# Kernel optimization log

Hardware: AMD Instinct MI355X
Metric: run time of the kernel (lower is better)

## Reference

```python
import jax, jax.numpy as jnp
import numpy as np
import math

B, S, D, H, FF, V, L = 8, 1024, 512, 8, 2048, 32000, 6
HD = D // H
EPS = 1e-6


def _positional_encoding(seq_len, d_model):
    pos = np.arange(seq_len, dtype=np.float32)[:, None]
    div = np.exp(np.arange(0, d_model, 2, dtype=np.float32) * (-math.log(10000.0) / d_model))
    pe = np.zeros((seq_len, d_model), dtype=np.float32)
    pe[:, 0::2] = np.sin(pos * div)
    pe[:, 1::2] = np.cos(pos * div)
    return jnp.asarray(pe)[None]  # [1, S, D]


def setup_inputs() -> dict:
    key = jax.random.key(0)
    ks = jax.random.split(key, 10)
    s = 0.02
    return {
        'tokens': jax.random.randint(ks[0], (B, S), 0, V, dtype=jnp.int32),
        'mask': jnp.ones((B, 1, 1, S), dtype=jnp.int32),
        'emb': jax.random.normal(ks[1], (V, D), jnp.float32) * s,
        'Wq': jax.random.normal(ks[2], (D, D), jnp.float32) * s,
        'bq': jnp.zeros((D,), jnp.float32),
        'Wk': jax.random.normal(ks[3], (D, D), jnp.float32) * s,
        'bk': jnp.zeros((D,), jnp.float32),
        'Wv': jax.random.normal(ks[4], (D, D), jnp.float32) * s,
        'bv': jnp.zeros((D,), jnp.float32),
        'Wo': jax.random.normal(ks[5], (D, D), jnp.float32) * s,
        'bo': jnp.zeros((D,), jnp.float32),
        'W1': jax.random.normal(ks[6], (D, FF), jnp.float32) * s,
        'b1': jnp.zeros((FF,), jnp.float32),
        'W2': jax.random.normal(ks[7], (FF, D), jnp.float32) * s,
        'b2': jnp.zeros((D,), jnp.float32),
        'ln_a1': jnp.ones((1,), jnp.float32),
        'ln_b1': jnp.zeros((1,), jnp.float32),
        'ln_a2': jnp.ones((1,), jnp.float32),
        'ln_b2': jnp.zeros((1,), jnp.float32),
    }


def _layernorm(x, alpha, bias):
    # custom LN from source: unbiased std (torch default), scalar alpha/bias,
    # eps added to std (not variance)
    mean = jnp.mean(x, axis=-1, keepdims=True)
    std = jnp.std(x, axis=-1, keepdims=True, ddof=1)
    return alpha * (x - mean) / (std + EPS) + bias


def reference(tokens, mask, emb, Wq, bq, Wk, bk, Wv, bv, Wo, bo,
              W1, b1, W2, b2, ln_a1, ln_b1, ln_a2, ln_b2):
    b, s = tokens.shape
    x = emb[tokens] * jnp.asarray(math.sqrt(D), emb.dtype)  # [B,S,D]
    x = x + _positional_encoding(s, D)
    neg = jnp.asarray(-1e9, x.dtype)
    scale = jnp.asarray(1.0 / math.sqrt(HD), x.dtype)
    # NOTE: source reuses the same EncoderBlock instance -> shared weights per layer
    for _ in range(L):
        # --- self-attention sublayer (pre-norm residual) ---
        h = _layernorm(x, ln_a1, ln_b1)
        q = (h @ Wq + bq).reshape(b, s, H, HD).transpose(0, 2, 1, 3)
        k = (h @ Wk + bk).reshape(b, s, H, HD).transpose(0, 2, 1, 3)
        v = (h @ Wv + bv).reshape(b, s, H, HD).transpose(0, 2, 1, 3)
        scores = jnp.einsum('bhqd,bhkd->bhqk', q, k) * scale
        scores = jnp.where(mask == 0, neg, scores)
        attn = jax.nn.softmax(scores, axis=-1)
        o = jnp.einsum('bhqk,bhkd->bhqd', attn, v)
        o = o.transpose(0, 2, 1, 3).reshape(b, s, D)
        x = x + (o @ Wo + bo)
        # --- feed-forward sublayer (pre-norm residual) ---
        h2 = _layernorm(x, ln_a2, ln_b2)
        x = x + (jax.nn.relu(h2 @ W1 + b1) @ W2 + b2)
    return x
```

## Files before the change

kernel.cpp:

```cpp
#include <hip/hip_runtime.h>
#include <hip/hip_bf16.h>
#include <math.h>

#define BB 8
#define SS 1024
#define DD 512
#define HH 8
#define FF 2048
#define LL 6
#define HD 64
#define MM (BB * SS)
#define EPS 1e-6f
#define QKVS 1536

typedef __attribute__((ext_vector_type(8))) short bf16x8;
typedef __attribute__((ext_vector_type(4))) float f32x4;

typedef __attribute__((address_space(1))) const unsigned int g_u32;
typedef __attribute__((address_space(3))) unsigned int l_u32;

__device__ __forceinline__ short f2bf(float f) {
    union { float f; unsigned u; } c; c.f = f;
    unsigned u = c.u;
    u += 0x7fff + ((u >> 16) & 1);
    return (short)(u >> 16);
}

__device__ __forceinline__ void gload_lds16(const void* g, void* l) {
    __builtin_amdgcn_global_load_lds((g_u32*)g, (l_u32*)l, 16, 0, 0);
}

__global__ __launch_bounds__(256) void embed_pe_kernel(
    const int* __restrict__ tokens, const float* __restrict__ emb,
    float* __restrict__ x)
{
    int idx = blockIdx.x * 256 + threadIdx.x;
    int d  = idx & (DD - 1);
    int bs = idx >> 9;
    int s  = bs & (SS - 1);
    int tok = tokens[bs];
    float val = emb[(size_t)tok * DD + d] * 22.62741699796952f;
    int i2 = d & ~1;
    float freq = expf((float)i2 * -0.017988946039015984f);
    float ang = (float)s * freq;
    val += (d & 1) ? cosf(ang) : sinf(ang);
    x[idx] = val;
}

__global__ __launch_bounds__(256) void wcvt_kernel(
    const float* __restrict__ W, short* __restrict__ Wt, int K, int N)
{
    __shared__ float tile[32][33];
    int n0 = blockIdx.x * 32, k0 = blockIdx.y * 32;
    int tx = threadIdx.x & 31, ty = threadIdx.x >> 5;
    #pragma unroll
    for (int i = 0; i < 4; ++i)
        tile[ty + i * 8][tx] = W[(size_t)(k0 + ty + i * 8) * N + n0 + tx];
    __syncthreads();
    #pragma unroll
    for (int i = 0; i < 4; ++i)
        Wt[(size_t)(n0 + ty + i * 8) * K + k0 + tx] = f2bf(tile[tx][ty + i * 8]);
}

__global__ __launch_bounds__(256) void bcat_kernel(
    const float* __restrict__ bq, const float* __restrict__ bk,
    const float* __restrict__ bv, float* __restrict__ out)
{
    int i = blockIdx.x * 256 + threadIdx.x;
    float v = (i < 512) ? bq[i] : (i < 1024 ? bk[i - 512] : bv[i - 1024]);
    out[i] = v;
}

__global__ __launch_bounds__(256) void ln_kernel(
    const float* __restrict__ x, short* __restrict__ y,
    const float* __restrict__ alpha_p, const float* __restrict__ beta_p)
{
    int t = threadIdx.x;
    int half = t >> 7, i = t & 127;
    int row = blockIdx.x * 2 + half;
    const float* xr = x + (size_t)row * DD;
    float4 v = *(const float4*)(xr + i * 4);

    __shared__ float red[8];
    float s = v.x + v.y + v.z + v.w;
    #pragma unroll
    for (int o = 32; o >= 1; o >>= 1) s += __shfl_xor(s, o, 64);
    int wv = t >> 6;
    if ((t & 63) == 0) red[wv] = s;
    __syncthreads();
    float mean = (red[half * 2] + red[half * 2 + 1]) * (1.0f / 512.0f);

    float d0 = v.x - mean, d1 = v.y - mean, d2 = v.z - mean, d3 = v.w - mean;
    float q = d0 * d0 + d1 * d1 + d2 * d2 + d3 * d3;
    #pragma unroll
    for (int o = 32; o >= 1; o >>= 1) q += __shfl_xor(q, o, 64);
    if ((t & 63) == 0) red[4 + wv] = q;
    __syncthreads();
    float var = (red[4 + half * 2] + red[5 + half * 2]) * (1.0f / 511.0f);
    float stdv = sqrtf(var);

    float alpha = alpha_p[0], beta = beta_p[0];
    float inv = alpha / (stdv + EPS);
    short4 ov;
    ov.x = f2bf(d0 * inv + beta); ov.y = f2bf(d1 * inv + beta);
    ov.z = f2bf(d2 * inv + beta); ov.w = f2bf(d3 * inv + beta);
    *(short4*)(y + (size_t)row * DD + i * 4) = ov;
}

template <int BN, bool RELU, bool RES, bool OUT_BF16>
__global__ __launch_bounds__(256) void gemm_mfma(
    const short* __restrict__ A, const short* __restrict__ Wt,
    const float* __restrict__ bias, const float* __restrict__ R,
    void* __restrict__ Cout, int M, int N, int K)
{
    __shared__ __align__(16) short As[128 * 64];
    __shared__ __align__(16) short Bs[BN * 64];

    constexpr int MI = (BN == 128) ? 4 : 2;
    constexpr int NI = 4;

    const int t = threadIdx.x;
    const int w = t >> 6, l = t & 63;
    const int l15 = l & 15, l4 = l >> 4;
    const int wrow = (BN == 128) ? (w >> 1) * 64 : w * 32;
    const int wcol = (BN == 128) ? (w & 1) * 64 : 0;

    const int m0 = blockIdx.y * 128, n0 = blockIdx.x * BN;

    f32x4 acc[MI][NI];
    #pragma unroll
    for (int mi = 0; mi < MI; ++mi)
        #pragma unroll
        for (int ni = 0; ni < NI; ++ni) acc[mi][ni] = (f32x4){0.f, 0.f, 0.f, 0.f};

    const int lrow = l >> 3;
    const int lcol = (l & 7) * 8;

    for (int k0 = 0; k0 < K; k0 += 64) {
        #pragma unroll
        for (int i = 0; i < 4; ++i) {
            int r0 = (w * 4 + i) * 8;
            gload_lds16(A + (size_t)(m0 + r0 + lrow) * K + k0 + lcol, &As[r0 * 64]);
        }
        #pragma unroll
        for (int i = 0; i < BN / 32; ++i) {
            int r0 = (w * (BN / 32) + i) * 8;
            gload_lds16(Wt + (size_t)(n0 + r0 + lrow) * K + k0 + lcol, &Bs[r0 * 64]);
        }
        __syncthreads();

        #pragma unroll
        for (int ks = 0; ks < 2; ++ks) {
            bf16x8 af[MI], bf_[NI];
            #pragma unroll
            for (int mi = 0; mi < MI; ++mi)
                af[mi] = *(const bf16x8*)&As[(wrow + mi * 16 + l15) * 64 + ks * 32 + l4 * 8];
            #pragma unroll
            for (int ni = 0; ni < NI; ++ni)
                bf_[ni] = *(const bf16x8*)&Bs[(wcol + ni * 16 + l15) * 64 + ks * 32 + l4 * 8];
            #pragma unroll
            for (int mi = 0; mi < MI; ++mi)
                #pragma unroll
                for (int ni = 0; ni < NI; ++ni)
                    acc[mi][ni] = __builtin_amdgcn_mfma_f32_16x16x32_bf16(
                        af[mi], bf_[ni], acc[mi][ni], 0, 0, 0);
        }
        __syncthreads();
    }

    #pragma unroll
    for (int mi = 0; mi < MI; ++mi) {
        #pragma unroll
        for (int ni = 0; ni < NI; ++ni) {
            int col = n0 + wcol + ni * 16 + l15;
            float bcol = bias[col];
            #pragma unroll
            for (int r = 0; r < 4; ++r) {
                int row = m0 + wrow + mi * 16 + l4 * 4 + r;
                float c = acc[mi][ni][r] + bcol;
                if (RES)  c += R[(size_t)row * N + col];
                if (RELU) c = fmaxf(c, 0.0f);
                if (OUT_BF16) ((short*)Cout)[(size_t)row * N + col] = f2bf(c);
                else          ((float*)Cout)[(size_t)row * N + col] = c;
            }
        }
    }
}

#define SWZ(row, col) (((row) * 64 + (col)) ^ (((row) & 7) << 3))

__global__ __launch_bounds__(512, 4) void attn_mfma_kernel(
    const short* __restrict__ qkv, const int* __restrict__ mask,
    short* __restrict__ o)
{
    __shared__ __align__(16) short Ks[64 * 64];
    __shared__ __align__(16) short Vt[64 * 64];
    __shared__ __align__(16) short Ps[8][16 * 64];

    const int qt = blockIdx.x;
    const int bh = blockIdx.y;
    const int b = bh >> 3, h = bh & 7;

    const int t = threadIdx.x;
    const int w = t >> 6;
    const int l = t & 63;
    const int l15 = l & 15, l4 = l >> 4;

    const short* kb = qkv + ((size_t)b * SS) * QKVS + 512 + h * HD;
    const short* vb = qkv + ((size_t)b * SS) * QKVS + 1024 + h * HD;
    const int*   mb = mask + (size_t)b * SS;
    const int qbase = qt * 128 + w * 16;

    bf16x8 qf[2];
    #pragma unroll
    for (int ks = 0; ks < 2; ++ks)
        qf[ks] = *(const bf16x8*)(qkv + ((size_t)b * SS + qbase + l15) * QKVS
                                  + h * HD + ks * 32 + l4 * 8);

    float m_run[4], l_run[4];
    f32x4 O[4];
    #pragma unroll
    for (int r = 0; r < 4; ++r) { m_run[r] = -1e30f; l_run[r] = 0.0f; }
    #pragma unroll
    for (int ds = 0; ds < 4; ++ds) O[ds] = (f32x4){0.f, 0.f, 0.f, 0.f};

    short* Pw = Ps[w];
    const int srow = t >> 3;
    const int scol = (t & 7) * 8;

    for (int kt = 0; kt < SS / 64; ++kt) {
        {
            bf16x8 kv = *(const bf16x8*)(kb + (size_t)(kt * 64 + srow) * QKVS + scol);
            *(bf16x8*)&Ks[SWZ(srow, scol)] = kv;
            bf16x8 vv = *(const bf16x8*)(vb + (size_t)(kt * 64 + srow) * QKVS + scol);
            #pragma unroll
            for (int j = 0; j < 8; ++j)
                Vt[SWZ(scol + j, srow)] = vv[j];
        }
        __syncthreads();

        f32x4 S[4];
        #pragma unroll
        for (int ku = 0; ku < 4; ++ku) S[ku] = (f32x4){0.f, 0.f, 0.f, 0.f};
        #pragma unroll
        for (int ks = 0; ks < 2; ++ks) {
            bf16x8 kf[4];
            #pragma unroll
            for (int ku = 0; ku < 4; ++ku)
                kf[ku] = *(const bf16x8*)&Ks[SWZ(l15 + 16 * ku, ks * 32 + l4 * 8)];
            #pragma unroll
            for (int ku = 0; ku < 4; ++ku)
                S[ku] = __builtin_amdgcn_mfma_f32_16x16x32_bf16(
                    qf[ks], kf[ku], S[ku], 0, 0, 0);
        }

        int mv[4];
        #pragma unroll
        for (int ku = 0; ku < 4; ++ku) mv[ku] = mb[kt * 64 + ku * 16 + l15];

        float p[4][4];
        #pragma unroll
        for (int ku = 0; ku < 4; ++ku)
            #pragma unroll
            for (int r = 0; r < 4; ++r) {
                float sv = S[ku][r] * 0.125f;
                p[ku][r] = (mv[ku] == 0) ? -1e9f : sv;
            }

        #pragma unroll
        for (int r = 0; r < 4; ++r) {
            float mx = fmaxf(fmaxf(p[0][r], p[1][r]), fmaxf(p[2][r], p[3][r]));
            mx = fmaxf(mx, __shfl_xor(mx, 1, 64));
            mx = fmaxf(mx, __shfl_xor(mx, 2, 64));
            mx = fmaxf(mx, __shfl_xor(mx, 4, 64));
            mx = fmaxf(mx, __shfl_xor(mx, 8, 64));
            float mnew = fmaxf(m_run[r], mx);
            float sc_old = __expf(m_run[r] - mnew);
            m_run[r] = mnew;
            float ps = 0.0f;
            #pragma unroll
            for (int ku = 0; ku < 4; ++ku) {
                float e = __expf(p[ku][r] - mnew);
                p[ku][r] = e;
                ps += e;
            }
            ps += __shfl_xor(ps, 1, 64);
            ps += __shfl_xor(ps, 2, 64);
            ps += __shfl_xor(ps, 4, 64);
            ps += __shfl_xor(ps, 8, 64);
            l_run[r] = l_run[r] * sc_old + ps;
            #pragma unroll
            for (int ds = 0; ds < 4; ++ds) O[ds][r] *= sc_old;
        }

        #pragma unroll
        for (int ku = 0; ku < 4; ++ku)
            #pragma unroll
            for (int r = 0; r < 4; ++r)
                Pw[SWZ(l4 * 4 + r, ku * 16 + l15)] = f2bf(p[ku][r]);

        #pragma unroll
        for (int ks = 0; ks < 2; ++ks) {
            bf16x8 vf[4];
            #pragma unroll
            for (int ds = 0; ds < 4; ++ds)
                vf[ds] = *(const bf16x8*)&Vt[SWZ(l15 + 16 * ds, ks * 32 + l4 * 8)];
            bf16x8 pf = *(const bf16x8*)&Pw[SWZ(l15, ks * 32 + l4 * 8)];
            #pragma unroll
            for (int ds = 0; ds < 4; ++ds)
                O[ds] = __builtin_amdgcn_mfma_f32_16x16x32_bf16(
                    pf, vf[ds], O[ds], 0, 0, 0);
        }
        __syncthreads();
    }

    #pragma unroll
    for (int r = 0; r < 4; ++r) {
        float inv = 1.0f / l_run[r];
        int qrow = qbase + l4 * 4 + r;
        short* orow = o + ((size_t)b * SS + qrow) * DD + h * HD;
        #pragma unroll
        for (int ds = 0; ds < 4; ++ds)
            orow[ds * 16 + l15] = f2bf(O[ds][r] * inv);
    }
}

extern "C" void kernel_launch(void* const* d_in, const int* in_sizes, int n_in,
                              void* d_out, int out_size, void* d_ws, size_t ws_size,
                              hipStream_t stream)
{
    const int*   tokens = (const int*)  d_in[0];
    const int*   mask   = (const int*)  d_in[1];
    const float* emb    = (const float*)d_in[2];
    const float* Wq     = (const float*)d_in[3];
    const float* bq     = (const float*)d_in[4];
    const float* Wk     = (const float*)d_in[5];
    const float* bk     = (const float*)d_in[6];
    const float* Wv     = (const float*)d_in[7];
    const float* bv     = (const float*)d_in[8];
    const float* Wo     = (const float*)d_in[9];
    const float* bo     = (const float*)d_in[10];
    const float* W1     = (const float*)d_in[11];
    const float* b1     = (const float*)d_in[12];
    const float* W2     = (const float*)d_in[13];
    const float* b2     = (const float*)d_in[14];
    const float* ln_a1  = (const float*)d_in[15];
    const float* ln_b1  = (const float*)d_in[16];
    const float* ln_a2  = (const float*)d_in[17];
    const float* ln_b2  = (const float*)d_in[18];

    float* x = (float*)d_out;

    char* p = (char*)d_ws;
    short* qkv  = (short*)p;  p += (size_t)MM * QKVS * 2;
    short* h    = (short*)p;  p += (size_t)MM * DD * 2;
    short* ff   = (short*)p;  p += (size_t)MM * FF * 2;
    short* Wqkvt= (short*)p;  p += (size_t)QKVS * DD * 2;
    short* Wot  = (short*)p;  p += (size_t)DD * DD * 2;
    short* W1t  = (short*)p;  p += (size_t)FF * DD * 2;
    short* W2t  = (short*)p;  p += (size_t)DD * FF * 2;
    float* bqkv = (float*)p;  p += QKVS * 4;

    embed_pe_kernel<<<(MM * DD) / 256, 256, 0, stream>>>(tokens, emb, x);

    wcvt_kernel<<<dim3(DD / 32, DD / 32), 256, 0, stream>>>(Wq, Wqkvt,            DD, DD);
    wcvt_kernel<<<dim3(DD / 32, DD / 32), 256, 0, stream>>>(Wk, Wqkvt + 512*512,  DD, DD);
    wcvt_kernel<<<dim3(DD / 32, DD / 32), 256, 0, stream>>>(Wv, Wqkvt + 1024*512, DD, DD);
    wcvt_kernel<<<dim3(DD / 32, DD / 32), 256, 0, stream>>>(Wo, Wot, DD, DD);
    wcvt_kernel<<<dim3(FF / 32, DD / 32), 256, 0, stream>>>(W1, W1t, DD, FF);
    wcvt_kernel<<<dim3(DD / 32, FF / 32), 256, 0, stream>>>(W2, W2t, FF, DD);
    bcat_kernel<<<QKVS / 256, 256, 0, stream>>>(bq, bk, bv, bqkv);

    dim3 gQKV(QKVS / 128, MM / 128);
    dim3 gO  (DD / 64,    MM / 128);
    dim3 gF1 (FF / 128,   MM / 128);
    dim3 gF2 (DD / 64,    MM / 128);
    dim3 gA  (SS / 128,   BB * HH);

    for (int layer = 0; layer < LL; ++layer) {
        ln_kernel<<<MM / 2, 256, 0, stream>>>(x, h, ln_a1, ln_b1);
        gemm_mfma<128, false, false, true><<<gQKV, 256, 0, stream>>>(
            h, Wqkvt, bqkv, nullptr, qkv, MM, QKVS, DD);
        attn_mfma_kernel<<<gA, 512, 0, stream>>>(qkv, mask, h);
        gemm_mfma<64, false, true, false><<<gO, 256, 0, stream>>>(
            h, Wot, bo, x, x, MM, DD, DD);

        ln_kernel<<<MM / 2, 256, 0, stream>>>(x, h, ln_a2, ln_b2);
        gemm_mfma<128, true, false, true><<<gF1, 256, 0, stream>>>(
            h, W1t, b1, nullptr, ff, MM, FF, DD);
        gemm_mfma<64, false, true, false><<<gF2, 256, 0, stream>>>(
            ff, W2t, b2, x, x, MM, DD, FF);
    }
}
```

Before: 1.407 ms.

## Rework attention LDS layout, V transpose via shuffles, and MFMA row-sum

The attention kernel moves from 512-thread blocks with 128 queries to 256-thread blocks with 64 queries, doubling the grid. The K/V tiles switch to a byte-addressed XOR swizzle that mixes two row bit-groups, meant to cut LDS bank conflicts. V is transposed with lane-pair shuffles and 32-bit packed LDS stores instead of scalar 16-bit scatters. The softmax row sum now comes from an MFMA against a ones vector on the bf16 P tile, replacing the shuffle reductions. This adds a small rounding difference because the sum uses bf16 P, and each K/V tile is loaded by twice as many blocks in total.

```diff
diff --git a/kernel.cpp b/kernel.cpp
--- a/kernel.cpp
+++ b/kernel.cpp
@@ -29,6 +29,8 @@
 __device__ __forceinline__ void gload_lds16(const void* g, void* l) {
     __builtin_amdgcn_global_load_lds((g_u32*)g, (l_u32*)l, 16, 0, 0);
 }
+
+#define SWZB(row, cb) (((row) * 128) + ((cb) ^ ((((row) & 7) ^ (((row) >> 3) & 7)) << 4)))
 
 __global__ __launch_bounds__(256) void embed_pe_kernel(
     const int* __restrict__ tokens, const float* __restrict__ emb,
@@ -187,15 +189,13 @@
     }
 }
 
-#define SWZ(row, col) (((row) * 64 + (col)) ^ (((row) & 7) << 3))
-
-__global__ __launch_bounds__(512, 4) void attn_mfma_kernel(
+__global__ __launch_bounds__(256) void attn_mfma_kernel(
     const short* __restrict__ qkv, const int* __restrict__ mask,
     short* __restrict__ o)
 {
-    __shared__ __align__(16) short Ks[64 * 64];
-    __shared__ __align__(16) short Vt[64 * 64];
-    __shared__ __align__(16) short Ps[8][16 * 64];
+    __shared__ __align__(16) char Ks[64 * 128];
+    __shared__ __align__(16) char Vt[64 * 128];
+    __shared__ __align__(16) char Ps[4][16 * 128];
 
     const int qt = blockIdx.x;
     const int bh = blockIdx.y;
@@ -205,11 +205,12 @@
     const int w = t >> 6;
     const int l = t & 63;
     const int l15 = l & 15, l4 = l >> 4;
+    const int l7 = l & 7,  l8 = l >> 3;
 
     const short* kb = qkv + ((size_t)b * SS) * QKVS + 512 + h * HD;
     const short* vb = qkv + ((size_t)b * SS) * QKVS + 1024 + h * HD;
     const int*   mb = mask + (size_t)b * SS;
-    const int qbase = qt * 128 + w * 16;
+    const int qbase = qt * 64 + w * 16;
 
     bf16x8 qf[2];
     #pragma unroll
@@ -217,6 +218,10 @@
         qf[ks] = *(const bf16x8*)(qkv + ((size_t)b * SS + qbase + l15) * QKVS
                                   + h * HD + ks * 32 + l4 * 8);
 
+    bf16x8 onesv;
+    #pragma unroll
+    for (int j = 0; j < 8; ++j) onesv[j] = (short)0x3F80;
+
     float m_run[4], l_run[4];
     f32x4 O[4];
     #pragma unroll
@@ -224,18 +229,38 @@
     #pragma unroll
     for (int ds = 0; ds < 4; ++ds) O[ds] = (f32x4){0.f, 0.f, 0.f, 0.f};
 
-    short* Pw = Ps[w];
-    const int srow = t >> 3;
-    const int scol = (t & 7) * 8;
+    char* Pw = Ps[w];
+    const int par = l & 1;
 
     for (int kt = 0; kt < SS / 64; ++kt) {
-        {
-            bf16x8 kv = *(const bf16x8*)(kb + (size_t)(kt * 64 + srow) * QKVS + scol);
-            *(bf16x8*)&Ks[SWZ(srow, scol)] = kv;
-            bf16x8 vv = *(const bf16x8*)(vb + (size_t)(kt * 64 + srow) * QKVS + scol);
-            #pragma unroll
-            for (int j = 0; j < 8; ++j)
-                Vt[SWZ(scol + j, srow)] = vv[j];
+        #pragma unroll
+        for (int c = 0; c < 2; ++c) {
+            int krow = (t >> 3) + 32 * c;
+            bf16x8 kv = *(const bf16x8*)(kb + (size_t)(kt * 64 + krow) * QKVS + l7 * 8);
+            *(bf16x8*)&Ks[SWZB(krow, l7 * 16)] = kv;
+        }
+        #pragma unroll
+        for (int s = 0; s < 2; ++s) {
+            int key = 16 * w + 8 * s + l7;
+            int d0  = 8 * l8;
+            int4 vv = *(const int4*)(vb + (size_t)(kt * 64 + key) * QKVS + d0);
+            int p0 = __shfl_xor(vv.x, 1, 64);
+            int p1 = __shfl_xor(vv.y, 1, 64);
+            int p2 = __shfl_xor(vv.z, 1, 64);
+            int p3 = __shfl_xor(vv.w, 1, 64);
+            int cb = (key & ~1) * 2;
+            int v0 = par ? (int)(((unsigned)p0 >> 16) | (vv.x & 0xFFFF0000))
+                         : ((vv.x & 0xFFFF) | (p0 << 16));
+            int v1 = par ? (int)(((unsigned)p1 >> 16) | (vv.y & 0xFFFF0000))
+                         : ((vv.y & 0xFFFF) | (p1 << 16));
+            int v2 = par ? (int)(((unsigned)p2 >> 16) | (vv.z & 0xFFFF0000))
+                         : ((vv.z & 0xFFFF) | (p2 << 16));
+            int v3 = par ? (int)(((unsigned)p3 >> 16) | (vv.w & 0xFFFF0000))
+                         : ((vv.w & 0xFFFF) | (p3 << 16));
+            *(int*)&Vt[SWZB(d0 + 0 + par, cb)] = v0;
+            *(int*)&Vt[SWZB(d0 + 2 + par, cb)] = v1;
+            *(int*)&Vt[SWZB(d0 + 4 + par, cb)] = v2;
+            *(int*)&Vt[SWZB(d0 + 6 + par, cb)] = v3;
         }
         __syncthreads();
 
@@ -247,7 +272,7 @@
             bf16x8 kf[4];
             #pragma unroll
             for (int ku = 0; ku < 4; ++ku)
-                kf[ku] = *(const bf16x8*)&Ks[SWZ(l15 + 16 * ku, ks * 32 + l4 * 8)];
+                kf[ku] = *(const bf16x8*)&Ks[SWZB(ku * 16 + l15, ks * 64 + l4 * 16)];
             #pragma unroll
             for (int ku = 0; ku < 4; ++ku)
                 S[ku] = __builtin_amdgcn_mfma_f32_16x16x32_bf16(
@@ -267,6 +292,7 @@
                 p[ku][r] = (mv[ku] == 0) ? -1e9f : sv;
             }
 
+        float sc_old[4];
         #pragma unroll
         for (int r = 0; r < 4; ++r) {
             float mx = fmaxf(fmaxf(p[0][r], p[1][r]), fmaxf(p[2][r], p[3][r]));
@@ -275,41 +301,43 @@
             mx = fmaxf(mx, __shfl_xor(mx, 4, 64));
             mx = fmaxf(mx, __shfl_xor(mx, 8, 64));
             float mnew = fmaxf(m_run[r], mx);
-            float sc_old = __expf(m_run[r] - mnew);
+            sc_old[r] = __expf(m_run[r] - mnew);
             m_run[r] = mnew;
-            float ps = 0.0f;
-            #pragma unroll
-            for (int ku = 0; ku < 4; ++ku) {
-                float e = __expf(p[ku][r] - mnew);
-                p[ku][r] = e;
-                ps += e;
-            }
-            ps += __shfl_xor(ps, 1, 64);
-            ps += __shfl_xor(ps, 2, 64);
-            ps += __shfl_xor(ps, 4, 64);
-            ps += __shfl_xor(ps, 8, 64);
-            l_run[r] = l_run[r] * sc_old + ps;
-            #pragma unroll
-            for (int ds = 0; ds < 4; ++ds) O[ds][r] *= sc_old;
+            #pragma unroll
+            for (int ku = 0; ku < 4; ++ku)
+                p[ku][r] = __expf(p[ku][r] - mnew);
+            #pragma unroll
+            for (int ds = 0; ds < 4; ++ds) O[ds][r] *= sc_old[r];
         }
 
         #pragma unroll
         for (int ku = 0; ku < 4; ++ku)
             #pragma unroll
             for (int r = 0; r < 4; ++r)
-                Pw[SWZ(l4 * 4 + r, ku * 16 + l15)] = f2bf(p[ku][r]);
+                *(short*)&Pw[SWZB(l4 * 4 + r, (ku * 16 + l15) * 2)] = f2bf(p[ku][r]);
+
+        bf16x8 pf[2];
+        #pragma unroll
+        for (int ks = 0; ks < 2; ++ks)
+            pf[ks] = *(const bf16x8*)&Pw[SWZB(l15, ks * 64 + l4 * 16)];
+
+        f32x4 rs = (f32x4){0.f, 0.f, 0.f, 0.f};
+        rs = __builtin_amdgcn_mfma_f32_16x16x32_bf16(pf[0], onesv, rs, 0, 0, 0);
+        rs = __builtin_amdgcn_mfma_f32_16x16x32_bf16(pf[1], onesv, rs, 0, 0, 0);
+        #pragma unroll
+        for (int r = 0; r < 4; ++r)
+            l_run[r] = l_run[r] * sc_old[r] + rs[r];
 
         #pragma unroll
         for (int ks = 0; ks < 2; ++ks) {
             bf16x8 vf[4];
             #pragma unroll
             for (int ds = 0; ds < 4; ++ds)
-                vf[ds] = *(const bf16x8*)&Vt[SWZ(l15 + 16 * ds, ks * 32 + l4 * 8)];
-            bf16x8 pf = *(const bf16x8*)&Pw[SWZ(l15, ks * 32 + l4 * 8)];
+                vf[ds] = *(const bf16x8*)&Vt[SWZB(ds * 16 + l15, ks * 64 + l4 * 16)];
             #pragma unroll
             for (int ds = 0; ds < 4; ++ds)
                 O[ds] = __builtin_amdgcn_mfma_f32_16x16x32_bf16(
-                    pf, vf[ds], O[ds], 0, 0, 0);
+                    pf[ks], vf[ds], O[ds], 0, 0, 0);
         }
         __syncthreads();
     }
@@ -375,13 +403,13 @@
     dim3 gO  (DD / 64,    MM / 128);
     dim3 gF1 (FF / 128,   MM / 128);
     dim3 gF2 (DD / 64,    MM / 128);
-    dim3 gA  (SS / 128,   BB * HH);
+    dim3 gA  (SS / 64,    BB * HH);
 
     for (int layer = 0; layer < LL; ++layer) {
         ln_kernel<<<MM / 2, 256, 0, stream>>>(x, h, ln_a1, ln_b1);
         gemm_mfma<128, false, false, true><<<gQKV, 256, 0, stream>>>(
             h, Wqkvt, bqkv, nullptr, qkv, MM, QKVS, DD);
-        attn_mfma_kernel<<<gA, 512, 0, stream>>>(qkv, mask, h);
+        attn_mfma_kernel<<<gA, 256, 0, stream>>>(qkv, mask, h);
         gemm_mfma<64, false, true, false><<<gO, 256, 0, stream>>>(
             h, Wot, bo, x, x, MM, DD, DD);
 
```

Result: slower. 1.487 ms (+5.7%).
